# Kernel optimization log

Measured on AMD Instinct MI355X. Metric: run time of the kernel, lower is better.

## Reference

```python
import jax, jax.numpy as jnp
import numpy as np

B, V, T = 8, 16, 64
DIN, H, RH, K, TMP = 6, 256, 64, 2, 256
E = V * (V - 1)
NREL, NPOS = 7, 3  # 2D relative / positional feature counts

_edges = np.ones((V, V)) - np.eye(V)
SEND = jnp.asarray(np.where(_edges)[0])
RECV = jnp.asarray(np.where(_edges)[1])


def _w(k, shape, fan):
    return jax.random.normal(k, shape, jnp.float32) / np.sqrt(fan)


def setup_inputs() -> dict:
    key = jax.random.key(0)
    ks = jax.random.split(key, 20)
    d = {}
    d['rel_feat'] = jax.random.normal(ks[0], (B, V, T, DIN), jnp.float32)
    d['edge_attr_raw'] = jax.random.normal(ks[1], (B, E, T, NREL + DIN), jnp.float32)
    d['edge_pos'] = jax.random.normal(ks[2], (B, E, T, NPOS), jnp.float32)
    d['ef_w1'] = _w(ks[3], (H, NREL + DIN + NPOS), NREL + DIN + NPOS); d['ef_b1'] = jnp.full((H,), 0.1)
    d['ef_w2'] = _w(ks[4], (H, H), H); d['ef_b2'] = jnp.full((H,), 0.1)
    d['res_w'] = _w(ks[5], (H, DIN), DIN); d['res_b'] = jnp.full((H,), 0.1)
    d['m3_w1'] = _w(ks[6], (H, H), H); d['m3_b1'] = jnp.full((H,), 0.1)
    d['m3_w2'] = _w(ks[7], (H, H), H); d['m3_b2'] = jnp.full((H,), 0.1)
    d['m4_w1'] = _w(ks[8], (H, 3 * H), 3 * H); d['m4_b1'] = jnp.full((H,), 0.1)
    d['m4_w2'] = _w(ks[9], (H, H), H); d['m4_b2'] = jnp.full((H,), 0.1)
    d['f_wih'] = _w(ks[10], (4 * RH, H), H); d['f_whh'] = _w(ks[11], (4 * RH, RH), RH)
    d['f_bih'] = jnp.zeros((4 * RH,)); d['f_bhh'] = jnp.zeros((4 * RH,))
    d['r_wih'] = _w(ks[12], (4 * RH, H), H); d['r_whh'] = _w(ks[13], (4 * RH, RH), RH)
    d['r_bih'] = jnp.zeros((4 * RH,)); d['r_bhh'] = jnp.zeros((4 * RH,))
    d['p_w'] = _w(ks[14], (K, RH), RH); d['p_b'] = jnp.full((K,), 0.1)
    d['e_w1'] = _w(ks[15], (TMP, 2 * RH), 2 * RH); d['e_b1'] = jnp.full((TMP,), 0.1)
    d['e_w2'] = _w(ks[16], (K, TMP), TMP); d['e_b2'] = jnp.full((K,), 0.1)
    return d


def _lstm(x, wih, whh, bih, bhh):
    # x: [N, T, H] -> hidden sequence [N, T, RH]; torch gate order i, f, g, o
    n = x.shape[0]
    rh = whh.shape[1]
    xw = jnp.einsum('nth,gh->ntg', x, wih) + bih  # input GEMM hoisted out of scan

    def step(carry, xt):
        h, c = carry
        z = xt + h @ whh.T + bhh
        i, f, g, o = jnp.split(z, 4, axis=-1)
        c = jax.nn.sigmoid(f) * c + jax.nn.sigmoid(i) * jnp.tanh(g)
        h = jax.nn.sigmoid(o) * jnp.tanh(c)
        return (h, c), h

    h0 = jnp.zeros((n, rh), x.dtype)
    _, hs = jax.lax.scan(step, (h0, h0), jnp.swapaxes(xw, 0, 1))
    return jnp.swapaxes(hs, 0, 1)


def reference(rel_feat, edge_attr_raw, edge_pos, ef_w1, ef_b1, ef_w2, ef_b2, res_w, res_b, m3_w1, m3_b1, m3_w2, m3_b2, m4_w1, m4_b1, m4_w2, m4_b2, f_wih, f_whh, f_bih, f_bhh, r_wih, r_whh, r_bih, r_bhh, p_w, p_b, e_w1, e_b1, e_w2, e_b2):
    elu = jax.nn.elu
    # edge filter MLP: [B,E,T,NREL+DIN+NPOS] -> [B,E,T,H]
    ein = jnp.concatenate([edge_attr_raw, edge_pos], -1)
    edge_attr = elu(elu(ein @ ef_w1.T + ef_b1) @ ef_w2.T + ef_b2)
    # edge2node: scatter-sum over recv indices, normalized by (V-1)
    agg = jax.ops.segment_sum(jnp.moveaxis(edge_attr, 1, 0), RECV, num_segments=V)
    x = jnp.moveaxis(agg, 0, 1) / (V - 1) + (rel_feat @ res_w.T + res_b)
    # mlp3 on node embeddings
    x = elu(elu(x @ m3_w1.T + m3_b1) @ m3_w2.T + m3_b2)
    # node2edge gather + skip-concat with previous edge features -> mlp4
    x = jnp.concatenate([x[:, SEND], x[:, RECV], edge_attr], -1)  # [B,E,T,3H]
    x = elu(elu(x @ m4_w1.T + m4_b1) @ m4_w2.T + m4_b2)  # [B,E,T,H]
    # bidirectional LSTM over time, per edge
    seq = x.reshape(B * E, T, H)
    fwd = _lstm(seq, f_wih, f_whh, f_bih, f_bhh)
    rev = jnp.flip(_lstm(jnp.flip(seq, 1), r_wih, r_whh, r_bih, r_bhh), 1)
    prior = (fwd @ p_w.T + p_b).reshape(B, E, T, K).transpose(0, 2, 1, 3)  # [B,T,E,K]
    comb = jnp.concatenate([fwd, rev], -1)
    enc = (elu(comb @ e_w1.T + e_b1) @ e_w2.T + e_b2).reshape(B, E, T, K).transpose(0, 2, 1, 3)
    return prior, enc
```

## Files before the change

### kernel.cpp

```cpp
#include <hip/hip_runtime.h>
#include <cstdint>
#include <cstddef>
#include <type_traits>

#define B_ 8
#define V_ 16
#define T_ 64
#define E_ 240
#define H_ 256
#define RH_ 64
#define K_ 2
#define DIN_ 6
#define BET_ (B_*E_*T_)
#define BVT_ (B_*V_*T_)
#define BE_ (B_*E_)

typedef unsigned short ushort_t;
typedef unsigned int u32;
typedef __attribute__((ext_vector_type(8))) short bf16x8;
typedef __attribute__((ext_vector_type(4))) float f32x4;

__device__ __forceinline__ float eluf(float x) { return x > 0.f ? x : __expf(x) - 1.f; }
__device__ __forceinline__ float fsig(float x) { return 1.f / (1.f + __expf(-x)); }
__device__ __forceinline__ float ftanh_(float x) {
    float y = fminf(fmaxf(x, -8.f), 8.f);
    float e = __expf(2.f * y);
    return (e - 1.f) / (e + 1.f);
}
__device__ __forceinline__ float b2f(ushort_t u) {
    union { float f; uint32_t i; } v; v.i = ((uint32_t)u) << 16; return v.f;
}
__device__ __forceinline__ ushort_t f2b(float f) {
    union { float f; uint32_t i; } v; v.f = f;
    uint32_t r = (v.i + 0x7FFFu + ((v.i >> 16) & 1u)) >> 16;
    return (ushort_t)r;
}

__device__ __forceinline__ void gll16(const void* g, void* l) {
    __builtin_amdgcn_global_load_lds(
        (const __attribute__((address_space(1))) u32*)g,
        (__attribute__((address_space(3))) u32*)l, 16, 0, 0);
}

template<int KD, int ACT>
__global__ __launch_bounds__(512, 2) void gemm8_k(
    const ushort_t* __restrict__ A, const ushort_t* __restrict__ Wt,
    const float* __restrict__ b1, const float* __restrict__ b2,
    ushort_t* __restrict__ C)
{
    __shared__ ushort_t lds[4][32][512];
    const int tid = threadIdx.x;
    const int lane = tid & 63;
    const int w = tid >> 6;
    const int wm = w >> 2, wn = w & 3;
    const int m0 = blockIdx.x * 256;
    const int r16 = lane & 15, kq = lane >> 4;
    constexpr int NH = KD / 32;

    const ushort_t* Ag0 = A + (size_t)(m0 + w * 16 + r16) * KD + kq * 8;
    const ushort_t* Ag1 = A + (size_t)(m0 + (w + 8) * 16 + r16) * KD + kq * 8;
    const ushort_t* Bg0 = Wt + (size_t)(w * 16 + r16) * KD + kq * 8;
    const ushort_t* Bg1 = Wt + (size_t)((w + 8) * 16 + r16) * KD + kq * 8;

    f32x4 acc[8][4];
    #pragma unroll
    for (int i = 0; i < 8; ++i)
        #pragma unroll
        for (int j = 0; j < 4; ++j)
            acc[i][j] = (f32x4){0.f, 0.f, 0.f, 0.f};

#define ST8(h) do { int sl_ = (h) & 3; int kk_ = (h) * 32;                  \
    gll16(Ag0 + kk_, &lds[sl_][w][0]);                                      \
    gll16(Ag1 + kk_, &lds[sl_][w + 8][0]);                                  \
    gll16(Bg0 + kk_, &lds[sl_][16 + w][0]);                                 \
    gll16(Bg1 + kk_, &lds[sl_][16 + w + 8][0]);                             \
} while (0)

    ST8(0); ST8(1); ST8(2);
    asm volatile("s_waitcnt vmcnt(8)" ::: "memory");
    __builtin_amdgcn_s_barrier();

    for (int h = 0; h < NH; ++h) {
        if (h + 3 < NH) ST8(h + 3);
        const int sl = h & 3;
        bf16x8 bfr[4];
        #pragma unroll
        for (int nf = 0; nf < 4; ++nf)
            bfr[nf] = *(const bf16x8*)&lds[sl][16 + wn * 4 + nf][lane * 8];
        #pragma unroll
        for (int mh = 0; mh < 2; ++mh) {
            bf16x8 af[4];
            #pragma unroll
            for (int mf = 0; mf < 4; ++mf)
                af[mf] = *(const bf16x8*)&lds[sl][wm * 8 + mh * 4 + mf][lane * 8];
            __builtin_amdgcn_s_setprio(1);
            #pragma unroll
            for (int mf = 0; mf < 4; ++mf)
                #pragma unroll
                for (int nf = 0; nf < 4; ++nf)
                    acc[mh * 4 + mf][nf] = __builtin_amdgcn_mfma_f32_16x16x32_bf16(
                        bfr[nf], af[mf], acc[mh * 4 + mf][nf], 0, 0, 0);
            __builtin_amdgcn_s_setprio(0);
        }
        asm volatile("s_waitcnt lgkmcnt(0)" ::: "memory");
        if (h < NH - 3)       { asm volatile("s_waitcnt vmcnt(8)" ::: "memory"); }
        else if (h == NH - 3) { asm volatile("s_waitcnt vmcnt(4)" ::: "memory"); }
        else if (h == NH - 2) { asm volatile("s_waitcnt vmcnt(0)" ::: "memory"); }
        if (h < NH - 1) __builtin_amdgcn_s_barrier();
    }
#undef ST8

    #pragma unroll
    for (int mi = 0; mi < 8; ++mi) {
        int mrow = m0 + wm * 128 + mi * 16 + r16;
        #pragma unroll
        for (int nf = 0; nf < 4; ++nf) {
            int nb = wn * 64 + nf * 16 + kq * 4;
            float4 bb = *(const float4*)&b1[nb];
            if (b2) {
                float4 b2v = *(const float4*)&b2[nb];
                bb.x += b2v.x; bb.y += b2v.y; bb.z += b2v.z; bb.w += b2v.w;
            }
            float v0 = acc[mi][nf][0] + bb.x;
            float v1 = acc[mi][nf][1] + bb.y;
            float v2 = acc[mi][nf][2] + bb.z;
            float v3 = acc[mi][nf][3] + bb.w;
            if (ACT) { v0 = eluf(v0); v1 = eluf(v1); v2 = eluf(v2); v3 = eluf(v3); }
            ushort4 o; o.x = f2b(v0); o.y = f2b(v1); o.z = f2b(v2); o.w = f2b(v3);
            *(ushort4*)&C[(size_t)mrow * 256 + nb] = o;
        }
    }
}

__global__ __launch_bounds__(256) void gemm_ein_k(
    const float* __restrict__ ear, const float* __restrict__ epos,
    const float* __restrict__ W, const float* __restrict__ b1,
    ushort_t* __restrict__ C)
{
    __shared__ float As[16][64];
    __shared__ float Ws[16][64];
    const int m0 = blockIdx.x * 64, n0 = blockIdx.y * 64;
    const int tid = threadIdx.x;
    const int tm = tid >> 4, tn = tid & 15;
    const int lm = tid >> 2, lq = tid & 3;
    const int m = m0 + lm;
    float a_[4];
    #pragma unroll
    for (int q = 0; q < 4; ++q) {
        int c = lq * 4 + q;
        a_[q] = (c < 13) ? ear[(size_t)m * 13 + c] : epos[(size_t)m * 3 + (c - 13)];
    }
    float4 wv = *(const float4*)(W + (size_t)(n0 + lm) * 16 + lq * 4);
    As[lq*4+0][lm] = a_[0]; As[lq*4+1][lm] = a_[1]; As[lq*4+2][lm] = a_[2]; As[lq*4+3][lm] = a_[3];
    Ws[lq*4+0][lm] = wv.x; Ws[lq*4+1][lm] = wv.y; Ws[lq*4+2][lm] = wv.z; Ws[lq*4+3][lm] = wv.w;
    __syncthreads();
    float acc[4][4] = {};
    #pragma unroll
    for (int k = 0; k < 16; ++k) {
        float4 a = *(const float4*)&As[k][tm * 4];
        float4 w = *(const float4*)&Ws[k][tn * 4];
        float aa[4] = {a.x, a.y, a.z, a.w};
        float ww[4] = {w.x, w.y, w.z, w.w};
        #pragma unroll
        for (int i = 0; i < 4; ++i)
            #pragma unroll
            for (int j = 0; j < 4; ++j)
                acc[i][j] += aa[i] * ww[j];
    }
    #pragma unroll
    for (int i = 0; i < 4; ++i) {
        ushort4 o;
        o.x = f2b(eluf(acc[i][0] + b1[n0 + tn*4 + 0]));
        o.y = f2b(eluf(acc[i][1] + b1[n0 + tn*4 + 1]));
        o.z = f2b(eluf(acc[i][2] + b1[n0 + tn*4 + 2]));
        o.w = f2b(eluf(acc[i][3] + b1[n0 + tn*4 + 3]));
        *(ushort4*)(C + (size_t)(m0 + tm * 4 + i) * H_ + (n0 + tn * 4)) = o;
    }
}

__global__ __launch_bounds__(512, 1) void gemm8_mlp3_k(
    const ushort_t* __restrict__ Xb, const ushort_t* __restrict__ w1,
    const float* __restrict__ b1, const ushort_t* __restrict__ w2,
    const float* __restrict__ b2, ushort_t* __restrict__ Out)
{
    __shared__ ushort_t H1[8][8][512];
    __shared__ ushort_t slots[36864];
    const int tid = threadIdx.x;
    const int lane = tid & 63;
    const int w = tid >> 6;
    const int m0 = blockIdx.x * 128;
    const int r16 = lane & 15, kq = lane >> 4;

    const ushort_t* Ag = Xb + (size_t)(m0 + w * 16 + r16) * 256 + kq * 8;
    const size_t bo0 = (size_t)(2 * w * 16 + r16) * 256 + kq * 8;
    const size_t bo1 = (size_t)((2 * w + 1) * 16 + r16) * 256 + kq * 8;

    float4 bb1[2], bb2[2];
    #pragma unroll
    for (int nf = 0; nf < 2; ++nf) {
        bb1[nf] = *(const float4*)&b1[w * 32 + nf * 16 + kq * 4];
        bb2[nf] = *(const float4*)&b2[w * 32 + nf * 16 + kq * 4];
    }

#define M3_ST0(h) do { int sl_ = (h) % 3;                                   \
    gll16(Ag + (h) * 32, &slots[sl_ * 12288 + w * 512]);                    \
    gll16(w1 + bo0 + (h) * 32, &slots[sl_ * 12288 + 4096 + 2 * w * 512]);   \
    gll16(w1 + bo1 + (h) * 32, &slots[sl_ * 12288 + 4096 + (2 * w + 1) * 512]); \
} while (0)
#define M3_ST1(h) do { int sl_ = (h) & 1; int kk_ = (h) * 32;               \
    gll16(w2 + bo0 + kk_, &slots[sl_ * 8192 + 2 * w * 512]);                \
    gll16(w2 + bo1 + kk_, &slots[sl_ * 8192 + (2 * w + 1) * 512]);          \
} while (0)

    f32x4 acc0[8][2];
    #pragma unroll
    for (int i = 0; i < 8; ++i) { acc0[i][0] = (f32x4){0,0,0,0}; acc0[i][1] = (f32x4){0,0,0,0}; }

    M3_ST0(0); M3_ST0(1);
    asm volatile("s_waitcnt vmcnt(3)" ::: "memory");
    __builtin_amdgcn_s_barrier();

    for (int h = 0; h < 8; ++h) {
        if (h + 2 < 8) M3_ST0(h + 2);
        const int sl = h % 3;
        bf16x8 af[8], bfr[2];
        #pragma unroll
        for (int mf = 0; mf < 8; ++mf)
            af[mf] = *(const bf16x8*)&slots[sl * 12288 + mf * 512 + lane * 8];
        #pragma unroll
        for (int nf = 0; nf < 2; ++nf)
            bfr[nf] = *(const bf16x8*)&slots[sl * 12288 + 4096 + (2 * w + nf) * 512 + lane * 8];
        #pragma unroll
        for (int mf = 0; mf < 8; ++mf)
            #pragma unroll
            for (int nf = 0; nf < 2; ++nf)
                acc0[mf][nf] = __builtin_amdgcn_mfma_f32_16x16x32_bf16(bfr[nf], af[mf], acc0[mf][nf], 0, 0, 0);
        asm volatile("s_waitcnt lgkmcnt(0)" ::: "memory");
        if (h <= 5)      { asm volatile("s_waitcnt vmcnt(3)" ::: "memory"); }
        else if (h == 6) { asm volatile("s_waitcnt vmcnt(0)" ::: "memory"); }
        if (h < 7) __builtin_amdgcn_s_barrier();
    }

    M3_ST1(0);
    #pragma unroll
    for (int mf = 0; mf < 8; ++mf) {
        #pragma unroll
        for (int nf = 0; nf < 2; ++nf) {
            ushort4 o;
            o.x = f2b(eluf(acc0[mf][nf][0] + bb1[nf].x));
            o.y = f2b(eluf(acc0[mf][nf][1] + bb1[nf].y));
            o.z = f2b(eluf(acc0[mf][nf][2] + bb1[nf].z));
            o.w = f2b(eluf(acc0[mf][nf][3] + bb1[nf].w));
            int lanew = r16 + 16 * ((nf << 1) | (kq >> 1));
            *(ushort4*)&H1[mf][w][lanew * 8 + (kq & 1) * 4] = o;
            acc0[mf][nf] = (f32x4){0.f, 0.f, 0.f, 0.f};
        }
    }
    asm volatile("s_waitcnt lgkmcnt(0)" ::: "memory");
    asm volatile("s_waitcnt vmcnt(0)" ::: "memory");
    __builtin_amdgcn_s_barrier();

    for (int h = 0; h < 8; ++h) {
        if (h + 1 < 8) M3_ST1(h + 1);
        const int sl = h & 1;
        bf16x8 af[8], bfr[2];
        #pragma unroll
        for (int mf = 0; mf < 8; ++mf)
            af[mf] = *(const bf16x8*)&H1[mf][h][lane * 8];
        #pragma unroll
        for (int nf = 0; nf < 2; ++nf)
            bfr[nf] = *(const bf16x8*)&slots[sl * 8192 + (2 * w + nf) * 512 + lane * 8];
        #pragma unroll
        for (int mf = 0; mf < 8; ++mf)
            #pragma unroll
            for (int nf = 0; nf < 2; ++nf)
                acc0[mf][nf] = __builtin_amdgcn_mfma_f32_16x16x32_bf16(bfr[nf], af[mf], acc0[mf][nf], 0, 0, 0);
        asm volatile("s_waitcnt lgkmcnt(0)" ::: "memory");
        if (h + 1 < 8) { asm volatile("s_waitcnt vmcnt(0)" ::: "memory"); }
        if (h < 7) __builtin_amdgcn_s_barrier();
    }

    #pragma unroll
    for (int mf = 0; mf < 8; ++mf) {
        int row = m0 + mf * 16 + r16;
        #pragma unroll
        for (int nf = 0; nf < 2; ++nf) {
            int col = w * 32 + nf * 16 + kq * 4;
            ushort4 o;
            o.x = f2b(eluf(acc0[mf][nf][0] + bb2[nf].x));
            o.y = f2b(eluf(acc0[mf][nf][1] + bb2[nf].y));
            o.z = f2b(eluf(acc0[mf][nf][2] + bb2[nf].z));
            o.w = f2b(eluf(acc0[mf][nf][3] + bb2[nf].w));
            *(ushort4*)&Out[(size_t)row * 256 + col] = o;
        }
    }
#undef M3_ST0
#undef M3_ST1
}

__global__ __launch_bounds__(512, 2) void gemm8_mlp4_k(
    const ushort_t* __restrict__ X2b, const ushort_t* __restrict__ EA,
    const ushort_t* __restrict__ Wt, const float* __restrict__ b1,
    ushort_t* __restrict__ C)
{
    __shared__ ushort_t lds[4][32][512];
    const int tid = threadIdx.x;
    const int lane = tid & 63;
    const int w = tid >> 6;
    const int wm = w >> 2, wn = w & 3;
    const int m0 = blockIdx.x * 256;
    const int r16 = lane & 15, kq = lane >> 4;
    constexpr int NH = 24;

    const ushort_t* AS[2]; const ushort_t* AR[2]; const ushort_t* AE[2];
    #pragma unroll
    for (int ff = 0; ff < 2; ++ff) {
        int f = w + ff * 8;
        int m = m0 + f * 16 + r16;
        int be = m >> 6, t = m & 63;
        int b = be / E_, e = be % E_;
        int s = e / (V_ - 1);
        int r0 = e % (V_ - 1);
        int rr = r0 + (r0 >= s ? 1 : 0);
        AS[ff] = X2b + ((size_t)((b * V_ + s) * T_ + t)) * H_ + kq * 8;
        AR[ff] = X2b + ((size_t)((b * V_ + rr) * T_ + t)) * H_ + kq * 8;
        AE[ff] = EA + (size_t)m * H_ + kq * 8;
    }
    const ushort_t* Bg0 = Wt + (size_t)(w * 16 + r16) * 768 + kq * 8;
    const ushort_t* Bg1 = Wt + (size_t)((w + 8) * 16 + r16) * 768 + kq * 8;

    f32x4 acc[8][4];
    #pragma unroll
    for (int i = 0; i < 8; ++i)
        #pragma unroll
        for (int j = 0; j < 4; ++j)
            acc[i][j] = (f32x4){0.f, 0.f, 0.f, 0.f};

#define STM(h) do { int sl_ = (h) & 3; int kk_ = (h) * 32;                  \
    int seg_ = kk_ >> 8, off_ = kk_ & 255;                                  \
    const ushort_t* a0_ = (seg_ == 0 ? AS[0] : seg_ == 1 ? AR[0] : AE[0]) + off_; \
    const ushort_t* a1_ = (seg_ == 0 ? AS[1] : seg_ == 1 ? AR[1] : AE[1]) + off_; \
    gll16(a0_, &lds[sl_][w][0]);                                            \
    gll16(a1_, &lds[sl_][w + 8][0]);                                        \
    gll16(Bg0 + kk_, &lds[sl_][16 + w][0]);                                 \
    gll16(Bg1 + kk_, &lds[sl_][16 + w + 8][0]);                             \
} while (0)

    STM(0); STM(1); STM(2);
    asm volatile("s_waitcnt vmcnt(8)" ::: "memory");
    __builtin_amdgcn_s_barrier();

    for (int h = 0; h < NH; ++h) {
        if (h + 3 < NH) STM(h + 3);
        const int sl = h & 3;
        bf16x8 bfr[4];
        #pragma unroll
        for (int nf = 0; nf < 4; ++nf)
            bfr[nf] = *(const bf16x8*)&lds[sl][16 + wn * 4 + nf][lane * 8];
        #pragma unroll
        for (int mh = 0; mh < 2; ++mh) {
            bf16x8 af[4];
            #pragma unroll
            for (int mf = 0; mf < 4; ++mf)
                af[mf] = *(const bf16x8*)&lds[sl][wm * 8 + mh * 4 + mf][lane * 8];
            __builtin_amdgcn_s_setprio(1);
            #pragma unroll
            for (int mf = 0; mf < 4; ++mf)
                #pragma unroll
                for (int nf = 0; nf < 4; ++nf)
                    acc[mh * 4 + mf][nf] = __builtin_amdgcn_mfma_f32_16x16x32_bf16(
                        bfr[nf], af[mf], acc[mh * 4 + mf][nf], 0, 0, 0);
            __builtin_amdgcn_s_setprio(0);
        }
        asm volatile("s_waitcnt lgkmcnt(0)" ::: "memory");
        if (h < NH - 3)       { asm volatile("s_waitcnt vmcnt(8)" ::: "memory"); }
        else if (h == NH - 3) { asm volatile("s_waitcnt vmcnt(4)" ::: "memory"); }
        else if (h == NH - 2) { asm volatile("s_waitcnt vmcnt(0)" ::: "memory"); }
        if (h < NH - 1) __builtin_amdgcn_s_barrier();
    }
#undef STM

    #pragma unroll
    for (int mi = 0; mi < 8; ++mi) {
        int mrow = m0 + wm * 128 + mi * 16 + r16;
        #pragma unroll
        for (int nf = 0; nf < 4; ++nf) {
            int nb = wn * 64 + nf * 16 + kq * 4;
            float4 bb = *(const float4*)&b1[nb];
            float v0 = eluf(acc[mi][nf][0] + bb.x);
            float v1 = eluf(acc[mi][nf][1] + bb.y);
            float v2 = eluf(acc[mi][nf][2] + bb.z);
            float v3 = eluf(acc[mi][nf][3] + bb.w);
            ushort4 o; o.x = f2b(v0); o.y = f2b(v1); o.z = f2b(v2); o.w = f2b(v3);
            *(ushort4*)&C[(size_t)mrow * 256 + nb] = o;
        }
    }
}

__global__ __launch_bounds__(256) void wconv_k(
    const float* __restrict__ ef_w2, const float* __restrict__ m4_w1,
    const float* __restrict__ m4_w2, const float* __restrict__ f_wih,
    const float* __restrict__ r_wih, const float* __restrict__ e_w1,
    const float* __restrict__ m3_w1, const float* __restrict__ m3_w2,
    ushort_t* __restrict__ Wb)
{
    int i = blockIdx.x * 256 + threadIdx.x;
    const float* src; int off;
    if (i < 65536)       { src = ef_w2; off = i; }
    else if (i < 262144) { src = m4_w1; off = i - 65536; }
    else if (i < 327680) { src = m4_w2; off = i - 262144; }
    else if (i < 393216) { src = f_wih; off = i - 327680; }
    else if (i < 458752) { src = r_wih; off = i - 393216; }
    else if (i < 491520) { src = e_w1;  off = i - 458752; }
    else if (i < 557056) { src = m3_w1; off = i - 491520; }
    else                 { src = m3_w2; off = i - 557056; }
    Wb[i] = f2b(src[off]);
}

__global__ __launch_bounds__(256) void e2n_k(
    const ushort_t* __restrict__ EA, const float* __restrict__ rel,
    const float* __restrict__ res_w, const float* __restrict__ res_b,
    ushort_t* __restrict__ X)
{
    const int idx = blockIdx.x;
    const int t = idx & (T_ - 1);
    const int bv = idx >> 6;
    const int v = bv & (V_ - 1);
    const int b = bv >> 4;
    const int h = threadIdx.x;
    float sum = 0.f;
    #pragma unroll
    for (int i = 0; i < V_; ++i) {
        if (i == v) continue;
        int jj = (v < i) ? v : v - 1;
        int e = i * (V_ - 1) + jj;
        sum += b2f(EA[(((size_t)(b * E_ + e)) * T_ + t) * H_ + h]);
    }
    const float* rp = rel + ((size_t)bv * T_ + t) * DIN_;
    float res = res_b[h];
    #pragma unroll
    for (int d = 0; d < DIN_; ++d) res += rp[d] * res_w[h * DIN_ + d];
    X[((size_t)bv * T_ + t) * H_ + h] = f2b(sum * (1.f / 15.f) + res);
}

__global__ __launch_bounds__(256) void lstm_mfma4_k(
    const ushort_t* __restrict__ Gf, const ushort_t* __restrict__ Gr,
    const float* __restrict__ whh_f, const float* __restrict__ whh_r,
    ushort_t* __restrict__ COMB)
{
    __shared__ ushort_t hlds[2][1024];
    const int dir = blockIdx.y;
    const ushort_t* G = dir ? Gr : Gf;
    const float* whh = dir ? whh_r : whh_f;
    const int tid = threadIdx.x;
    const int lane = tid & 63;
    const int w = tid >> 6;
    const int seq = lane & 15, kq = lane >> 4;
    const int be0 = blockIdx.x * 16;
    const int swz = (seq & 7) << 4;

    bf16x8 wf[4][2];
    #pragma unroll
    for (int a = 0; a < 4; ++a) {
        #pragma unroll
        for (int ks = 0; ks < 2; ++ks) {
            const float* p = whh + (size_t)((a * 4 + w) * 16 + seq) * 64 + ks * 32 + kq * 8;
            float4 x0 = *(const float4*)p;
            float4 x1 = *(const float4*)(p + 4);
            bf16x8 v;
            v[0] = (short)f2b(x0.x); v[1] = (short)f2b(x0.y);
            v[2] = (short)f2b(x0.z); v[3] = (short)f2b(x0.w);
            v[4] = (short)f2b(x1.x); v[5] = (short)f2b(x1.y);
            v[6] = (short)f2b(x1.z); v[7] = (short)f2b(x1.w);
            wf[a][ks] = v;
        }
    }

    const ushort_t* grow = G + ((size_t)(be0 + seq) * T_) * 256 + kq * 4;
    ushort_t* crow = COMB + ((size_t)(be0 + seq) * T_) * 128 + (dir ? 64 : 0) + 16 * w + 4 * kq;

    float c[4] = {};
    ushort4 gx[4];
    const int t0 = dir ? (T_ - 1) : 0;
    #pragma unroll
    for (int a = 0; a < 4; ++a)
        gx[a] = *(const ushort4*)(grow + (size_t)t0 * 256 + (a * 4 + w) * 16);

    for (int s = 0; s < T_; ++s) {
        const int t = dir ? (T_ - 1 - s) : s;
        f32x4 acc[4];
        #pragma unroll
        for (int a = 0; a < 4; ++a) {
            ushort4 g = gx[a];
            acc[a] = (f32x4){b2f(g.x), b2f(g.y), b2f(g.z), b2f(g.w)};
        }
        if (s < T_ - 1) {
            const int tn = dir ? (T_ - 2 - s) : (s + 1);
            #pragma unroll
            for (int a = 0; a < 4; ++a)
                gx[a] = *(const ushort4*)(grow + (size_t)tn * 256 + (a * 4 + w) * 16);
        }
        if (s) {
            bf16x8 af[2];
            #pragma unroll
            for (int ks = 0; ks < 2; ++ks) {
                int boff = (seq * 128 + ks * 64 + kq * 16) ^ swz;
                af[ks] = *(const bf16x8*)((const char*)hlds[(s - 1) & 1] + boff);
            }
            #pragma unroll
            for (int a = 0; a < 4; ++a) {
                acc[a] = __builtin_amdgcn_mfma_f32_16x16x32_bf16(wf[a][0], af[0], acc[a], 0, 0, 0);
                acc[a] = __builtin_amdgcn_mfma_f32_16x16x32_bf16(wf[a][1], af[1], acc[a], 0, 0, 0);
            }
        }
        float hh[4];
        #pragma unroll
        for (int r = 0; r < 4; ++r) {
            float zi = acc[0][r], zf = acc[1][r], zg = acc[2][r], zo = acc[3][r];
            float cc = fsig(zf) * c[r] + fsig(zi) * ftanh_(zg);
            c[r] = cc;
            hh[r] = fsig(zo) * ftanh_(cc);
        }
        ushort4 hv;
        hv.x = f2b(hh[0]); hv.y = f2b(hh[1]); hv.z = f2b(hh[2]); hv.w = f2b(hh[3]);
        int wb = (seq * 128 + 32 * w + 8 * kq) ^ swz;
        *(ushort4*)((char*)hlds[s & 1] + wb) = hv;
        *(ushort4*)(crow + (size_t)t * 128) = hv;
        asm volatile("s_waitcnt lgkmcnt(0)" ::: "memory");
        __builtin_amdgcn_sched_barrier(0);
        __builtin_amdgcn_s_barrier();
    }
}

__global__ __launch_bounds__(256) void prior_k(
    const ushort_t* __restrict__ COMB, const float* __restrict__ p_w,
    const float* __restrict__ p_b, float* __restrict__ out)
{
    const int row = blockIdx.x * 4 + (threadIdx.x >> 6);
    const int lane = threadIdx.x & 63;
    float hf = b2f(COMB[(size_t)row * 128 + lane]);
    float v0 = hf * p_w[lane];
    float v1 = hf * p_w[64 + lane];
    #pragma unroll
    for (int off = 32; off > 0; off >>= 1) {
        v0 += __shfl_down(v0, off, 64);
        v1 += __shfl_down(v1, off, 64);
    }
    if (lane == 0) {
        int t = row & (T_ - 1);
        int be = row >> 6;
        int e = be % E_, b = be / E_;
        size_t o = (((size_t)b * T_ + t) * E_ + e) * K_;
        out[o] = v0 + p_b[0];
        out[o + 1] = v1 + p_b[1];
    }
}

__global__ __launch_bounds__(512) void fused_enc_k(
    const ushort_t* __restrict__ COMB, const ushort_t* __restrict__ w_e1,
    const float* __restrict__ e_b1, const float* __restrict__ e_w2,
    const float* __restrict__ e_b2, float* __restrict__ out)
{
    __shared__ ushort_t sA[2][8][512];
    __shared__ ushort_t sW[2][16][512];
    __shared__ float part[128][4][2];
    const int tid = threadIdx.x;
    const int lane = tid & 63;
    const int w = tid >> 6;
    const int wr = w >> 2, wc = w & 3;
    const int m0 = blockIdx.x * 128;
    const int r16 = lane & 15, kq = lane >> 4;

    const ushort_t* Asrc = COMB + (size_t)(m0 + w * 16 + r16) * 128 + kq * 8;
    const size_t woffA = (size_t)((2 * w) * 16 + r16) * 128 + kq * 8;
    const size_t woffB = (size_t)((2 * w + 1) * 16 + r16) * 128 + kq * 8;

    float4 w2v[2][4];
    #pragma unroll
    for (int j = 0; j < 2; ++j)
        #pragma unroll
        for (int nf = 0; nf < 4; ++nf)
            w2v[j][nf] = *(const float4*)&e_w2[j * 256 + wc * 64 + nf * 16 + kq * 4];

    f32x4 acc[4][4];
    #pragma unroll
    for (int i = 0; i < 4; ++i)
        #pragma unroll
        for (int j = 0; j < 4; ++j)
            acc[i][j] = (f32x4){0.f, 0.f, 0.f, 0.f};

#define FE_STAGE(bufi, kt_) do {                                             \
    gll16(Asrc + (kt_) * 32, &sA[bufi][w][0]);                               \
    gll16(w_e1 + woffA + (kt_) * 32, &sW[bufi][2 * w][0]);                   \
    gll16(w_e1 + woffB + (kt_) * 32, &sW[bufi][2 * w + 1][0]);               \
} while (0)

    FE_STAGE(0, 0);
    asm volatile("s_waitcnt vmcnt(0)" ::: "memory");
    __builtin_amdgcn_s_barrier();

    for (int s = 0; s < 4; ++s) {
        const int buf = s & 1;
        if (s < 3) FE_STAGE(buf ^ 1, s + 1);
        bf16x8 af[4], bfr[4];
        #pragma unroll
        for (int mf = 0; mf < 4; ++mf)
            af[mf] = *(const bf16x8*)&sA[buf][wr * 4 + mf][lane * 8];
        #pragma unroll
        for (int nf = 0; nf < 4; ++nf)
            bfr[nf] = *(const bf16x8*)&sW[buf][wc * 4 + nf][lane * 8];
        #pragma unroll
        for (int mf = 0; mf < 4; ++mf)
            #pragma unroll
            for (int nf = 0; nf < 4; ++nf)
                acc[mf][nf] = __builtin_amdgcn_mfma_f32_16x16x32_bf16(bfr[nf], af[mf], acc[mf][nf], 0, 0, 0);
        asm volatile("s_waitcnt vmcnt(0)" ::: "memory");
        __builtin_amdgcn_s_barrier();
    }

    #pragma unroll
    for (int mf = 0; mf < 4; ++mf) {
        float s0 = 0.f, s1 = 0.f;
        #pragma unroll
        for (int nf = 0; nf < 4; ++nf) {
            int col = wc * 64 + nf * 16 + kq * 4;
            float4 bb = *(const float4*)&e_b1[col];
            float v0 = eluf(acc[mf][nf][0] + bb.x);
            float v1 = eluf(acc[mf][nf][1] + bb.y);
            float v2 = eluf(acc[mf][nf][2] + bb.z);
            float v3 = eluf(acc[mf][nf][3] + bb.w);
            s0 += v0 * w2v[0][nf].x + v1 * w2v[0][nf].y + v2 * w2v[0][nf].z + v3 * w2v[0][nf].w;
            s1 += v0 * w2v[1][nf].x + v1 * w2v[1][nf].y + v2 * w2v[1][nf].z + v3 * w2v[1][nf].w;
        }
        s0 += __shfl_xor(s0, 16, 64); s0 += __shfl_xor(s0, 32, 64);
        s1 += __shfl_xor(s1, 16, 64); s1 += __shfl_xor(s1, 32, 64);
        if (kq == 0) {
            part[wr * 64 + mf * 16 + r16][wc][0] = s0;
            part[wr * 64 + mf * 16 + r16][wc][1] = s1;
        }
    }
    __syncthreads();
    if (tid < 256) {
        int row = tid >> 1, k = tid & 1;
        float v = part[row][0][k] + part[row][1][k] + part[row][2][k] + part[row][3][k] + e_b2[k];
        int gr = m0 + row;
        int be = gr >> 6, t = gr & 63;
        int e = be % E_, b = be / E_;
        out[(size_t)(B_ * T_ * E_ * K_) + (((size_t)b * T_ + t) * E_ + e) * K_ + k] = v;
    }
#undef FE_STAGE
}

extern "C" void kernel_launch(void* const* d_in, const int* in_sizes, int n_in,
                              void* d_out, int out_size, void* d_ws, size_t ws_size,
                              hipStream_t stream)
{
    const float* rel    = (const float*)d_in[0];
    const float* ear    = (const float*)d_in[1];
    const float* epos   = (const float*)d_in[2];
    const float* ef_w1  = (const float*)d_in[3];
    const float* ef_b1  = (const float*)d_in[4];
    const float* ef_w2  = (const float*)d_in[5];
    const float* ef_b2  = (const float*)d_in[6];
    const float* res_w  = (const float*)d_in[7];
    const float* res_b  = (const float*)d_in[8];
    const float* m3_w1  = (const float*)d_in[9];
    const float* m3_b1  = (const float*)d_in[10];
    const float* m3_w2  = (const float*)d_in[11];
    const float* m3_b2  = (const float*)d_in[12];
    const float* m4_w1  = (const float*)d_in[13];
    const float* m4_b1  = (const float*)d_in[14];
    const float* m4_w2  = (const float*)d_in[15];
    const float* m4_b2  = (const float*)d_in[16];
    const float* f_wih  = (const float*)d_in[17];
    const float* f_whh  = (const float*)d_in[18];
    const float* f_bih  = (const float*)d_in[19];
    const float* f_bhh  = (const float*)d_in[20];
    const float* r_wih  = (const float*)d_in[21];
    const float* r_whh  = (const float*)d_in[22];
    const float* r_bih  = (const float*)d_in[23];
    const float* r_bhh  = (const float*)d_in[24];
    const float* p_w    = (const float*)d_in[25];
    const float* p_b    = (const float*)d_in[26];
    const float* e_w1   = (const float*)d_in[27];
    const float* e_b1   = (const float*)d_in[28];
    const float* e_w2   = (const float*)d_in[29];
    const float* e_b2   = (const float*)d_in[30];
    float* out = (float*)d_out;

    char* ws = (char*)d_ws;
    const size_t BIGB  = (size_t)BET_ * H_ * sizeof(ushort_t);
    const size_t COMBB = (size_t)BET_ * 128 * sizeof(ushort_t);
    const size_t X2BB  = (size_t)BVT_ * H_ * sizeof(ushort_t);
    ushort_t* R1   = (ushort_t*)(ws);
    ushort_t* R2   = (ushort_t*)(ws + BIGB);
    ushort_t* COMB = (ushort_t*)(ws + 2 * BIGB);
    ushort_t* X2b  = (ushort_t*)(ws + 2 * BIGB + COMBB);
    ushort_t* Wb   = (ushort_t*)(ws + 2 * BIGB + COMBB + X2BB);
    ushort_t* Xbf = (ushort_t*)(ws);
    const ushort_t* wb_ef2  = Wb + 0;
    const ushort_t* wb_m41  = Wb + 65536;
    const ushort_t* wb_m42  = Wb + 262144;
    const ushort_t* wb_fwih = Wb + 327680;
    const ushort_t* wb_rwih = Wb + 393216;
    const ushort_t* wb_ew1  = Wb + 458752;
    const ushort_t* wb_m31  = Wb + 491520;
    const ushort_t* wb_m32  = Wb + 557056;

    dim3 blk(256);
    dim3 blk8(512);
    dim3 g128(BET_ / 128);
    dim3 g256(BET_ / 256);
    dim3 gE64(BET_ / 64, 4);

    wconv_k<<<2432, blk, 0, stream>>>(ef_w2, m4_w1, m4_w2, f_wih, r_wih, e_w1, m3_w1, m3_w2, Wb);
    gemm_ein_k<<<gE64, blk, 0, stream>>>(ear, epos, ef_w1, ef_b1, R1);
    gemm8_k<256, 1><<<g256, blk8, 0, stream>>>(R1, wb_ef2, ef_b2, nullptr, R2);
    e2n_k<<<BVT_, blk, 0, stream>>>(R2, rel, res_w, res_b, Xbf);
    gemm8_mlp3_k<<<BVT_ / 128, blk8, 0, stream>>>(Xbf, wb_m31, m3_b1, wb_m32, m3_b2, X2b);
    gemm8_mlp4_k<<<g256, blk8, 0, stream>>>(X2b, R2, wb_m41, m4_b1, R1);
    gemm8_k<256, 1><<<g256, blk8, 0, stream>>>(R1, wb_m42, m4_b2, nullptr, R2);
    gemm8_k<256, 0><<<g256, blk8, 0, stream>>>(R2, wb_fwih, f_bih, f_bhh, R1);
    gemm8_k<256, 0><<<g256, blk8, 0, stream>>>(R2, wb_rwih, r_bih, r_bhh, R2);
    lstm_mfma4_k<<<dim3(BE_ / 16, 2), blk, 0, stream>>>(R1, R2, f_whh, r_whh, COMB);
    prior_k<<<BET_ / 4, blk, 0, stream>>>(COMB, p_w, p_b, out);
    fused_enc_k<<<g128, blk8, 0, stream>>>(COMB, wb_ew1, e_b1, e_w2, e_b2, out);
}
```

Measured before the change: 414.8 us.

## Double GEMM block to 16 waves with 512-row tiles and 3-stage LDS pipeline

The bf16 MFMA GEMM kernels, including the gathered mlp4 GEMM, now run 1024-thread blocks. Each block covers 512 rows instead of 256, so every weight tile staged in LDS is reused across twice as many rows. The LDS ring drops from four stages to three so the larger A tile still fits, with a matching prefetch depth and waitcnt schedule. This halves weight traffic per row and doubles waves per CU. In exchange, the grid shrinks to about one block per CU, pipelining is shallower, and the (1024,4) launch bounds may squeeze registers and cause spills.

After: 1.345 ms. +224.3%, slower.

```diff
diff --git a/kernel.cpp b/kernel.cpp
--- a/kernel.cpp
+++ b/kernel.cpp
@@ -43,24 +43,23 @@
 }
 
 template<int KD, int ACT>
-__global__ __launch_bounds__(512, 2) void gemm8_k(
+__global__ __launch_bounds__(1024, 4) void gemm16_k(
     const ushort_t* __restrict__ A, const ushort_t* __restrict__ Wt,
     const float* __restrict__ b1, const float* __restrict__ b2,
     ushort_t* __restrict__ C)
 {
-    __shared__ ushort_t lds[4][32][512];
+    __shared__ ushort_t lds[3][48][512];
     const int tid = threadIdx.x;
     const int lane = tid & 63;
     const int w = tid >> 6;
     const int wm = w >> 2, wn = w & 3;
-    const int m0 = blockIdx.x * 256;
+    const int m0 = blockIdx.x * 512;
     const int r16 = lane & 15, kq = lane >> 4;
     constexpr int NH = KD / 32;
 
     const ushort_t* Ag0 = A + (size_t)(m0 + w * 16 + r16) * KD + kq * 8;
-    const ushort_t* Ag1 = A + (size_t)(m0 + (w + 8) * 16 + r16) * KD + kq * 8;
-    const ushort_t* Bg0 = Wt + (size_t)(w * 16 + r16) * KD + kq * 8;
-    const ushort_t* Bg1 = Wt + (size_t)((w + 8) * 16 + r16) * KD + kq * 8;
+    const ushort_t* Ag1 = A + (size_t)(m0 + (w + 16) * 16 + r16) * KD + kq * 8;
+    const ushort_t* Bg  = Wt + (size_t)(w * 16 + r16) * KD + kq * 8;
 
     f32x4 acc[8][4];
     #pragma unroll
@@ -69,24 +68,23 @@
         for (int j = 0; j < 4; ++j)
             acc[i][j] = (f32x4){0.f, 0.f, 0.f, 0.f};
 
-#define ST8(h) do { int sl_ = (h) & 3; int kk_ = (h) * 32;                  \
+#define ST16(h) do { int sl_ = (h) % 3; int kk_ = (h) * 32;                 \
     gll16(Ag0 + kk_, &lds[sl_][w][0]);                                      \
-    gll16(Ag1 + kk_, &lds[sl_][w + 8][0]);                                  \
-    gll16(Bg0 + kk_, &lds[sl_][16 + w][0]);                                 \
-    gll16(Bg1 + kk_, &lds[sl_][16 + w + 8][0]);                             \
+    gll16(Ag1 + kk_, &lds[sl_][w + 16][0]);                                 \
+    gll16(Bg + kk_, &lds[sl_][32 + w][0]);                                  \
 } while (0)
 
-    ST8(0); ST8(1); ST8(2);
-    asm volatile("s_waitcnt vmcnt(8)" ::: "memory");
+    ST16(0); ST16(1);
+    asm volatile("s_waitcnt vmcnt(3)" ::: "memory");
     __builtin_amdgcn_s_barrier();
 
     for (int h = 0; h < NH; ++h) {
-        if (h + 3 < NH) ST8(h + 3);
-        const int sl = h & 3;
+        if (h + 2 < NH) ST16(h + 2);
+        const int sl = h % 3;
         bf16x8 bfr[4];
         #pragma unroll
         for (int nf = 0; nf < 4; ++nf)
-            bfr[nf] = *(const bf16x8*)&lds[sl][16 + wn * 4 + nf][lane * 8];
+            bfr[nf] = *(const bf16x8*)&lds[sl][32 + wn * 4 + nf][lane * 8];
         #pragma unroll
         for (int mh = 0; mh < 2; ++mh) {
             bf16x8 af[4];
@@ -103,12 +101,11 @@
             __builtin_amdgcn_s_setprio(0);
         }
         asm volatile("s_waitcnt lgkmcnt(0)" ::: "memory");
-        if (h < NH - 3)       { asm volatile("s_waitcnt vmcnt(8)" ::: "memory"); }
-        else if (h == NH - 3) { asm volatile("s_waitcnt vmcnt(4)" ::: "memory"); }
+        if (h <= NH - 3)      { asm volatile("s_waitcnt vmcnt(3)" ::: "memory"); }
         else if (h == NH - 2) { asm volatile("s_waitcnt vmcnt(0)" ::: "memory"); }
         if (h < NH - 1) __builtin_amdgcn_s_barrier();
     }
-#undef ST8
+#undef ST16
 
     #pragma unroll
     for (int mi = 0; mi < 8; ++mi) {
@@ -132,6 +129,102 @@
     }
 }
 
+__global__ __launch_bounds__(1024, 4) void gemm16_mlp4_k(
+    const ushort_t* __restrict__ X2b, const ushort_t* __restrict__ EA,
+    const ushort_t* __restrict__ Wt, const float* __restrict__ b1,
+    ushort_t* __restrict__ C)
+{
+    __shared__ ushort_t lds[3][48][512];
+    const int tid = threadIdx.x;
+    const int lane = tid & 63;
+    const int w = tid >> 6;
+    const int wm = w >> 2, wn = w & 3;
+    const int m0 = blockIdx.x * 512;
+    const int r16 = lane & 15, kq = lane >> 4;
+    constexpr int NH = 24;
+
+    const ushort_t* AS[2]; const ushort_t* AR[2]; const ushort_t* AE[2];
+    #pragma unroll
+    for (int ff = 0; ff < 2; ++ff) {
+        int f = w + ff * 16;
+        int m = m0 + f * 16 + r16;
+        int be = m >> 6, t = m & 63;
+        int b = be / E_, e = be % E_;
+        int s = e / (V_ - 1);
+        int r0 = e % (V_ - 1);
+        int rr = r0 + (r0 >= s ? 1 : 0);
+        AS[ff] = X2b + ((size_t)((b * V_ + s) * T_ + t)) * H_ + kq * 8;
+        AR[ff] = X2b + ((size_t)((b * V_ + rr) * T_ + t)) * H_ + kq * 8;
+        AE[ff] = EA + (size_t)m * H_ + kq * 8;
+    }
+    const ushort_t* Bg = Wt + (size_t)(w * 16 + r16) * 768 + kq * 8;
+
+    f32x4 acc[8][4];
+    #pragma unroll
+    for (int i = 0; i < 8; ++i)
+        #pragma unroll
+        for (int j = 0; j < 4; ++j)
+            acc[i][j] = (f32x4){0.f, 0.f, 0.f, 0.f};
+
+#define STM16(h) do { int sl_ = (h) % 3; int kk_ = (h) * 32;                \
+    int seg_ = kk_ >> 8, off_ = kk_ & 255;                                  \
+    const ushort_t* a0_ = (seg_ == 0 ? AS[0] : seg_ == 1 ? AR[0] : AE[0]) + off_; \
+    const ushort_t* a1_ = (seg_ == 0 ? AS[1] : seg_ == 1 ? AR[1] : AE[1]) + off_; \
+    gll16(a0_, &lds[sl_][w][0]);                                            \
+    gll16(a1_, &lds[sl_][w + 16][0]);                                       \
+    gll16(Bg + kk_, &lds[sl_][32 + w][0]);                                  \
+} while (0)
+
+    STM16(0); STM16(1);
+    asm volatile("s_waitcnt vmcnt(3)" ::: "memory");
+    __builtin_amdgcn_s_barrier();
+
+    for (int h = 0; h < NH; ++h) {
+        if (h + 2 < NH) STM16(h + 2);
+        const int sl = h % 3;
+        bf16x8 bfr[4];
+        #pragma unroll
+        for (int nf = 0; nf < 4; ++nf)
+            bfr[nf] = *(const bf16x8*)&lds[sl][32 + wn * 4 + nf][lane * 8];
+        #pragma unroll
+        for (int mh = 0; mh < 2; ++mh) {
+            bf16x8 af[4];
+            #pragma unroll
+            for (int mf = 0; mf < 4; ++mf)
+                af[mf] = *(const bf16x8*)&lds[sl][wm * 8 + mh * 4 + mf][lane * 8];
+            __builtin_amdgcn_s_setprio(1);
+            #pragma unroll
+            for (int mf = 0; mf < 4; ++mf)
+                #pragma unroll
+                for (int nf = 0; nf < 4; ++nf)
+                    acc[mh * 4 + mf][nf] = __builtin_amdgcn_mfma_f32_16x16x32_bf16(
+                        bfr[nf], af[mf], acc[mh * 4 + mf][nf], 0, 0, 0);
+            __builtin_amdgcn_s_setprio(0);
+        }
+        asm volatile("s_waitcnt lgkmcnt(0)" ::: "memory");
+        if (h <= NH - 3)      { asm volatile("s_waitcnt vmcnt(3)" ::: "memory"); }
+        else if (h == NH - 2) { asm volatile("s_waitcnt vmcnt(0)" ::: "memory"); }
+        if (h < NH - 1) __builtin_amdgcn_s_barrier();
+    }
+#undef STM16
+
+    #pragma unroll
+    for (int mi = 0; mi < 8; ++mi) {
+        int mrow = m0 + wm * 128 + mi * 16 + r16;
+        #pragma unroll
+        for (int nf = 0; nf < 4; ++nf) {
+            int nb = wn * 64 + nf * 16 + kq * 4;
+            float4 bb = *(const float4*)&b1[nb];
+            float v0 = eluf(acc[mi][nf][0] + bb.x);
+            float v1 = eluf(acc[mi][nf][1] + bb.y);
+            float v2 = eluf(acc[mi][nf][2] + bb.z);
+            float v3 = eluf(acc[mi][nf][3] + bb.w);
+            ushort4 o; o.x = f2b(v0); o.y = f2b(v1); o.z = f2b(v2); o.w = f2b(v3);
+            *(ushort4*)&C[(size_t)mrow * 256 + nb] = o;
+        }
+    }
+}
+
 __global__ __launch_bounds__(256) void gemm_ein_k(
     const float* __restrict__ ear, const float* __restrict__ epos,
     const float* __restrict__ W, const float* __restrict__ b1,
@@ -296,105 +389,6 @@
     }
 #undef M3_ST0
 #undef M3_ST1
-}
-
-__global__ __launch_bounds__(512, 2) void gemm8_mlp4_k(
-    const ushort_t* __restrict__ X2b, const ushort_t* __restrict__ EA,
-    const ushort_t* __restrict__ Wt, const float* __restrict__ b1,
-    ushort_t* __restrict__ C)
-{
-    __shared__ ushort_t lds[4][32][512];
-    const int tid = threadIdx.x;
-    const int lane = tid & 63;
-    const int w = tid >> 6;
-    const int wm = w >> 2, wn = w & 3;
-    const int m0 = blockIdx.x * 256;
-    const int r16 = lane & 15, kq = lane >> 4;
-    constexpr int NH = 24;
-
-    const ushort_t* AS[2]; const ushort_t* AR[2]; const ushort_t* AE[2];
-    #pragma unroll
-    for (int ff = 0; ff < 2; ++ff) {
-        int f = w + ff * 8;
-        int m = m0 + f * 16 + r16;
-        int be = m >> 6, t = m & 63;
-        int b = be / E_, e = be % E_;
-        int s = e / (V_ - 1);
-        int r0 = e % (V_ - 1);
-        int rr = r0 + (r0 >= s ? 1 : 0);
-        AS[ff] = X2b + ((size_t)((b * V_ + s) * T_ + t)) * H_ + kq * 8;
-        AR[ff] = X2b + ((size_t)((b * V_ + rr) * T_ + t)) * H_ + kq * 8;
-        AE[ff] = EA + (size_t)m * H_ + kq * 8;
-    }
-    const ushort_t* Bg0 = Wt + (size_t)(w * 16 + r16) * 768 + kq * 8;
-    const ushort_t* Bg1 = Wt + (size_t)((w + 8) * 16 + r16) * 768 + kq * 8;
-
-    f32x4 acc[8][4];
-    #pragma unroll
-    for (int i = 0; i < 8; ++i)
-        #pragma unroll
-        for (int j = 0; j < 4; ++j)
-            acc[i][j] = (f32x4){0.f, 0.f, 0.f, 0.f};
-
-#define STM(h) do { int sl_ = (h) & 3; int kk_ = (h) * 32;                  \
-    int seg_ = kk_ >> 8, off_ = kk_ & 255;                                  \
-    const ushort_t* a0_ = (seg_ == 0 ? AS[0] : seg_ == 1 ? AR[0] : AE[0]) + off_; \
-    const ushort_t* a1_ = (seg_ == 0 ? AS[1] : seg_ == 1 ? AR[1] : AE[1]) + off_; \
-    gll16(a0_, &lds[sl_][w][0]);                                            \
-    gll16(a1_, &lds[sl_][w + 8][0]);                                        \
-    gll16(Bg0 + kk_, &lds[sl_][16 + w][0]);                                 \
-    gll16(Bg1 + kk_, &lds[sl_][16 + w + 8][0]);                             \
-} while (0)
-
-    STM(0); STM(1); STM(2);
-    asm volatile("s_waitcnt vmcnt(8)" ::: "memory");
-    __builtin_amdgcn_s_barrier();
-
-    for (int h = 0; h < NH; ++h) {
-        if (h + 3 < NH) STM(h + 3);
-        const int sl = h & 3;
-        bf16x8 bfr[4];
-        #pragma unroll
-        for (int nf = 0; nf < 4; ++nf)
-            bfr[nf] = *(const bf16x8*)&lds[sl][16 + wn * 4 + nf][lane * 8];
-        #pragma unroll
-        for (int mh = 0; mh < 2; ++mh) {
-            bf16x8 af[4];
-            #pragma unroll
-            for (int mf = 0; mf < 4; ++mf)
-                af[mf] = *(const bf16x8*)&lds[sl][wm * 8 + mh * 4 + mf][lane * 8];
-            __builtin_amdgcn_s_setprio(1);
-            #pragma unroll
-            for (int mf = 0; mf < 4; ++mf)
-                #pragma unroll
-                for (int nf = 0; nf < 4; ++nf)
-                    acc[mh * 4 + mf][nf] = __builtin_amdgcn_mfma_f32_16x16x32_bf16(
-                        bfr[nf], af[mf], acc[mh * 4 + mf][nf], 0, 0, 0);
-            __builtin_amdgcn_s_setprio(0);
-        }
-        asm volatile("s_waitcnt lgkmcnt(0)" ::: "memory");
-        if (h < NH - 3)       { asm volatile("s_waitcnt vmcnt(8)" ::: "memory"); }
-        else if (h == NH - 3) { asm volatile("s_waitcnt vmcnt(4)" ::: "memory"); }
-        else if (h == NH - 2) { asm volatile("s_waitcnt vmcnt(0)" ::: "memory"); }
-        if (h < NH - 1) __builtin_amdgcn_s_barrier();
-    }
-#undef STM
-
-    #pragma unroll
-    for (int mi = 0; mi < 8; ++mi) {
-        int mrow = m0 + wm * 128 + mi * 16 + r16;
-        #pragma unroll
-        for (int nf = 0; nf < 4; ++nf) {
-            int nb = wn * 64 + nf * 16 + kq * 4;
-            float4 bb = *(const float4*)&b1[nb];
-            float v0 = eluf(acc[mi][nf][0] + bb.x);
-            float v1 = eluf(acc[mi][nf][1] + bb.y);
-            float v2 = eluf(acc[mi][nf][2] + bb.z);
-            float v3 = eluf(acc[mi][nf][3] + bb.w);
-            ushort4 o; o.x = f2b(v0); o.y = f2b(v1); o.z = f2b(v2); o.w = f2b(v3);
-            *(ushort4*)&C[(size_t)mrow * 256 + nb] = o;
-        }
-    }
 }
 
 __global__ __launch_bounds__(256) void wconv_k(
@@ -709,19 +703,20 @@
 
     dim3 blk(256);
     dim3 blk8(512);
+    dim3 blk16(1024);
     dim3 g128(BET_ / 128);
-    dim3 g256(BET_ / 256);
+    dim3 g512(BET_ / 512);
     dim3 gE64(BET_ / 64, 4);
 
     wconv_k<<<2432, blk, 0, stream>>>(ef_w2, m4_w1, m4_w2, f_wih, r_wih, e_w1, m3_w1, m3_w2, Wb);
     gemm_ein_k<<<gE64, blk, 0, stream>>>(ear, epos, ef_w1, ef_b1, R1);
-    gemm8_k<256, 1><<<g256, blk8, 0, stream>>>(R1, wb_ef2, ef_b2, nullptr, R2);
+    gemm16_k<256, 1><<<g512, blk16, 0, stream>>>(R1, wb_ef2, ef_b2, nullptr, R2);
     e2n_k<<<BVT_, blk, 0, stream>>>(R2, rel, res_w, res_b, Xbf);
     gemm8_mlp3_k<<<BVT_ / 128, blk8, 0, stream>>>(Xbf, wb_m31, m3_b1, wb_m32, m3_b2, X2b);
-    gemm8_mlp4_k<<<g256, blk8, 0, stream>>>(X2b, R2, wb_m41, m4_b1, R1);
-    gemm8_k<256, 1><<<g256, blk8, 0, stream>>>(R1, wb_m42, m4_b2, nullptr, R2);
-    gemm8_k<256, 0><<<g256, blk8, 0, stream>>>(R2, wb_fwih, f_bih, f_bhh, R1);
-    gemm8_k<256, 0><<<g256, blk8, 0, stream>>>(R2, wb_rwih, r_bih, r_bhh, R2);
+    gemm16_mlp4_k<<<g512, blk16, 0, stream>>>(X2b, R2, wb_m41, m4_b1, R1);
+    gemm16_k<256, 1><<<g512, blk16, 0, stream>>>(R1, wb_m42, m4_b2, nullptr, R2);
+    gemm16_k<256, 0><<<g512, blk16, 0, stream>>>(R2, wb_fwih, f_bih, f_bhh, R1);
+    gemm16_k<256, 0><<<g512, blk16, 0, stream>>>(R2, wb_rwih, r_bih, r_bhh, R2);
     lstm_mfma4_k<<<dim3(BE_ / 16, 2), blk, 0, stream>>>(R1, R2, f_whh, r_whh, COMB);
     prior_k<<<BET_ / 4, blk, 0, stream>>>(COMB, p_w, p_b, out);
     fused_enc_k<<<g128, blk8, 0, stream>>>(COMB, wb_ew1, e_b1, e_w2, e_b2, out);
```
